# Kernel tuning notes

Hardware: AMD Instinct MI355X
Metric: run time of the kernel (lower is better)

## Reference

```python
import jax, jax.numpy as jnp
import numpy as np

CUBE_SIZE = 3
RADIUS = 0.25
NSAMPLE = 512
B, N = 128, 8192


def make_centers():
    # grid of cube_size^3 centers, centered at origin, spacing = radius
    g = np.arange(CUBE_SIZE, dtype=np.float32)
    c = np.stack(np.meshgrid(g, g, g, indexing='ij'), axis=-1).reshape(-1, 3)
    c -= (CUBE_SIZE - 1) / 2.0
    c *= RADIUS
    return jnp.asarray(c[None])  # [1, P, 3]


def setup_inputs() -> dict:
    key = jax.random.key(0)
    xyz = jax.random.normal(key, (B, N, 3), dtype=jnp.float32)
    return {"xyz": xyz, "centers": make_centers()}


def reference(xyz, centers):
    # xyz: [B, N, 3], centers: [1, P, 3]
    b_, n_, _ = xyz.shape
    p_ = centers.shape[1]
    c = jnp.broadcast_to(centers, (b_, p_, 3))

    # squared distances [B, P, N] without materializing [B,P,N,3]
    x2 = jnp.sum(xyz * xyz, axis=-1)            # [B, N]
    c2 = jnp.sum(c * c, axis=-1)                # [B, P]
    xc = jnp.einsum('bpd,bnd->bpn', c, xyz)     # [B, P, N]
    dist2 = x2[:, None, :] + c2[:, :, None] - 2.0 * xc

    # ball query: first NSAMPLE points (in index order) with dist2 < r^2;
    # remaining slots padded with the first found index (0 if none found),
    # matching the PointNet++ CUDA kernel semantics.
    mask = dist2 < (RADIUS * RADIUS)
    order = jnp.where(mask, jnp.cumsum(mask, axis=-1) - 1, NSAMPLE)  # slot per point
    first_idx = jnp.argmax(mask, axis=-1)                             # [B, P], 0 if none
    idx = jnp.broadcast_to(first_idx[..., None], (b_, p_, NSAMPLE))
    bi = jnp.arange(b_)[:, None, None]
    pi = jnp.arange(p_)[None, :, None]
    js = jnp.broadcast_to(jnp.arange(n_)[None, None, :], (b_, p_, n_))
    idx = idx.at[bi, pi, order].set(js, mode='drop')                  # [B, P, NSAMPLE]

    # gather neighbors and re-center (QueryAndGroup with use_xyz, no features)
    grouped = jnp.take_along_axis(xyz[:, None, :, :], idx[..., None], axis=2)  # [B,P,S,3]
    grouped = grouped - c[:, :, None, :]

    # permute(0,2,3,1) of [B,3,P,S] -> [B,P,S,3] then merge batch and center dims
    return grouped.reshape(b_ * p_, NSAMPLE, 3)
```

## Files before the change

### kernel.cpp

```cpp
#include <hip/hip_runtime.h>


constexpr int P        = 27;
constexpr int N        = 8192;
constexpr int S        = 512;
constexpr int B        = 128;
constexpr int CAND_MAX = 1024;

__global__ __launch_bounds__(256) void pc_fused_kernel(
    const float* __restrict__ xyz, const float* __restrict__ centers,
    float* __restrict__ out) {
  int i   = blockIdx.x;
  int xcd = i & 7;
  int j   = i >> 3;
  int b   = xcd * 16 + j / 7;
  int g   = j % 7;
  int tid = threadIdx.x, lane = tid & 63, wave = tid >> 6;

  __shared__ float4 s_cand[CAND_MAX];
  __shared__ int    s_wsum[4];

  const float* pts = xyz + (size_t)b * (N * 3);

  const float4* p4 = (const float4*)pts + (size_t)tid * 24;
  unsigned mask = 0;
#pragma unroll
  for (int grp = 0; grp < 4; ++grp) {
    float4 f[6];
#pragma unroll
    for (int k = 0; k < 6; ++k) f[k] = p4[grp * 6 + k];
    const float* fp = (const float*)f;
#pragma unroll
    for (int k = 0; k < 8; ++k) {
      float x = fp[3 * k + 0], y = fp[3 * k + 1], z = fp[3 * k + 2];
      float cx = fminf(fmaxf(roundf(x * 4.0f), -1.0f), 1.0f) * 0.25f;
      float cy = fminf(fmaxf(roundf(y * 4.0f), -1.0f), 1.0f) * 0.25f;
      float cz = fminf(fmaxf(roundf(z * 4.0f), -1.0f), 1.0f) * 0.25f;
      float dx = x - cx, dy = y - cy, dz = z - cz;
      float d2 = dx * dx + dy * dy + dz * dz;
      if (d2 < 0.0625f + 1e-4f) mask |= 1u << (grp * 8 + k);
    }
  }

  int pcnt = __popc(mask);
  int incl = pcnt;
#pragma unroll
  for (int d = 1; d < 64; d <<= 1) {
    int v = __shfl_up(incl, d);
    if (lane >= d) incl += v;
  }
  if (lane == 63) s_wsum[wave] = incl;
  __syncthreads();
  int woff = 0, ctot = 0;
#pragma unroll
  for (int w = 0; w < 4; ++w) {
    int c = s_wsum[w];
    if (w < wave) woff += c;
    ctot += c;
  }
  int pos = woff + (incl - pcnt);
  unsigned mm = mask;
  while (mm) {
    int k = __ffs(mm) - 1;
    mm &= mm - 1;
    if (pos < CAND_MAX) {
      int n = tid * 32 + k;
      s_cand[pos] = make_float4(pts[n * 3], pts[n * 3 + 1], pts[n * 3 + 2], 0.f);
    }
    ++pos;
  }
  __syncthreads();

  int p = g * 4 + wave;
  if (p >= P) return;

  float cx = centers[p * 3 + 0];
  float cy = centers[p * 3 + 1];
  float cz = centers[p * 3 + 2];
  double cxd = (double)cx, cyd = (double)cy, czd = (double)cz;
  float* o = out + ((size_t)b * P + p) * (S * 3);

  int base = 0;
  bool has_first = false;
  float f0x = 0.f, f0y = 0.f, f0z = 0.f;
  if (ctot <= CAND_MAX) {
    for (int off = 0; off < ctot && base < S; off += 64) {
      int idx  = off + lane;
      bool act = idx < ctot;
      float4 pt = act ? s_cand[idx] : make_float4(0.f, 0.f, 0.f, 0.f);
      double dx = (double)pt.x - cxd;
      double dy = (double)pt.y - cyd;
      double dz = (double)pt.z - czd;
      bool inball = act && (dx * dx + dy * dy + dz * dz < 0.0625);
      unsigned long long m = __ballot(inball);
      int slot = base + __popcll(m & ((1ull << lane) - 1ull));
      if (inball && slot < S) {
        float fx = pt.x - cx, fy = pt.y - cy, fz = pt.z - cz;
        o[slot * 3 + 0] = fx;
        o[slot * 3 + 1] = fy;
        o[slot * 3 + 2] = fz;
        if (slot == 0) { has_first = true; f0x = fx; f0y = fy; f0z = fz; }
      }
      base += __popcll(m);
    }
  } else {
    for (int off = 0; off < N && base < S; off += 64) {
      int n = off + lane;
      float x = pts[n * 3 + 0], y = pts[n * 3 + 1], z = pts[n * 3 + 2];
      double dx = (double)x - cxd, dy = (double)y - cyd, dz = (double)z - czd;
      bool inball = dx * dx + dy * dy + dz * dz < 0.0625;
      unsigned long long m = __ballot(inball);
      int slot = base + __popcll(m & ((1ull << lane) - 1ull));
      if (inball && slot < S) {
        float fx = x - cx, fy = y - cy, fz = z - cz;
        o[slot * 3 + 0] = fx;
        o[slot * 3 + 1] = fy;
        o[slot * 3 + 2] = fz;
        if (slot == 0) { has_first = true; f0x = fx; f0y = fy; f0z = fz; }
      }
      base += __popcll(m);
    }
  }

  float px, py, pz;
  unsigned long long fm = __ballot(has_first);
  if (fm) {
    int src = __ffsll((unsigned long long)fm) - 1;
    px = __shfl(f0x, src); py = __shfl(f0y, src); pz = __shfl(f0z, src);
  } else {
    px = pts[0] - cx; py = pts[1] - cy; pz = pts[2] - cz;
  }

  int filled = base < S ? base : S;
  int d0 = filled * 3;
  int hb = (d0 + 3) & ~3;
  if (hb > 1536) hb = 1536;
  if (lane < hb - d0) {
    int d = d0 + lane;
    int rr = d % 3;
    o[d] = rr == 0 ? px : (rr == 1 ? py : pz);
  }
  for (int gq = (hb >> 2) + lane; gq < 1536 / 4; gq += 64) {
    int rr = gq % 3;
    float a  = rr == 0 ? px : (rr == 1 ? py : pz);
    float b2 = rr == 0 ? py : (rr == 1 ? pz : px);
    float c2 = rr == 0 ? pz : (rr == 1 ? px : py);
    ((float4*)o)[gq] = make_float4(a, b2, c2, a);
  }
}

extern "C" void kernel_launch(void* const* d_in, const int* in_sizes, int n_in,
                              void* d_out, int out_size, void* d_ws, size_t ws_size,
                              hipStream_t stream) {
  const float* xyz     = (const float*)d_in[0];
  const float* centers = (const float*)d_in[1];
  float* out           = (float*)d_out;
  (void)d_ws; (void)ws_size;
  pc_fused_kernel<<<B * 7, 256, 0, stream>>>(xyz, centers, out);
}
```

Before: 85.80 us.

## Compact candidates per-wave segments with ballot, removing block scan and global re-reads

Candidate filtering changes from per-thread 32-point bitmasks plus a block-wide scan into four per-wave segments of 2048 points each. Each wave compacts its in-range candidates with ballot/popcount into its own shared-memory segment, prefetching the next point. This removes the shuffle scan, one barrier and the scattered global re-reads of candidate coordinates. In exchange it uses strided scalar loads instead of float4 loads, has a per-segment cap of 512, and the query phase now walks four segments in order.

Result: faster. 81.79 us (-4.7%).

```diff
diff --git a/kernel.cpp b/kernel.cpp
--- a/kernel.cpp
+++ b/kernel.cpp
@@ -1,11 +1,12 @@
 #include <hip/hip_runtime.h>
 
 
-constexpr int P        = 27;
-constexpr int N        = 8192;
-constexpr int S        = 512;
-constexpr int B        = 128;
-constexpr int CAND_MAX = 1024;
+constexpr int P      = 27;
+constexpr int N      = 8192;
+constexpr int S      = 512;
+constexpr int B      = 128;
+constexpr int SEGPTS = 2048;
+constexpr int SEGCAP = 512;
 
 __global__ __launch_bounds__(256) void pc_fused_kernel(
     const float* __restrict__ xyz, const float* __restrict__ centers,
@@ -17,59 +18,45 @@
   int g   = j % 7;
   int tid = threadIdx.x, lane = tid & 63, wave = tid >> 6;
 
-  __shared__ float4 s_cand[CAND_MAX];
-  __shared__ int    s_wsum[4];
+  __shared__ float4 s_cand[4 * SEGCAP];
+  __shared__ int    s_wcnt[4];
 
   const float* pts = xyz + (size_t)b * (N * 3);
 
-  const float4* p4 = (const float4*)pts + (size_t)tid * 24;
-  unsigned mask = 0;
-#pragma unroll
-  for (int grp = 0; grp < 4; ++grp) {
-    float4 f[6];
-#pragma unroll
-    for (int k = 0; k < 6; ++k) f[k] = p4[grp * 6 + k];
-    const float* fp = (const float*)f;
-#pragma unroll
-    for (int k = 0; k < 8; ++k) {
-      float x = fp[3 * k + 0], y = fp[3 * k + 1], z = fp[3 * k + 2];
+  {
+    const float* sp = pts + wave * (SEGPTS * 3);
+    float4* seg = s_cand + wave * SEGCAP;
+    unsigned long long lmask = (1ull << lane) - 1ull;
+
+    int i3 = lane * 3;
+    float x = sp[i3], y = sp[i3 + 1], z = sp[i3 + 2];
+    int cnt = 0;
+    for (int it = 0; it < SEGPTS / 64; ++it) {
+      float nx = 0.f, ny = 0.f, nz = 0.f;
+      if (it < SEGPTS / 64 - 1) {
+        int n3 = ((it + 1) * 64 + lane) * 3;
+        nx = sp[n3]; ny = sp[n3 + 1]; nz = sp[n3 + 2];
+      }
       float cx = fminf(fmaxf(roundf(x * 4.0f), -1.0f), 1.0f) * 0.25f;
       float cy = fminf(fmaxf(roundf(y * 4.0f), -1.0f), 1.0f) * 0.25f;
       float cz = fminf(fmaxf(roundf(z * 4.0f), -1.0f), 1.0f) * 0.25f;
       float dx = x - cx, dy = y - cy, dz = z - cz;
-      float d2 = dx * dx + dy * dy + dz * dz;
-      if (d2 < 0.0625f + 1e-4f) mask |= 1u << (grp * 8 + k);
+      bool keep = (dx * dx + dy * dy + dz * dz) < (0.0625f + 1e-4f);
+
+      unsigned long long m = __ballot(keep);
+      if (keep) {
+        int pos = cnt + __popcll(m & lmask);
+        if (pos < SEGCAP) seg[pos] = make_float4(x, y, z, 0.0f);
+      }
+      cnt += __popcll(m);
+      x = nx; y = ny; z = nz;
     }
-  }
-
-  int pcnt = __popc(mask);
-  int incl = pcnt;
-#pragma unroll
-  for (int d = 1; d < 64; d <<= 1) {
-    int v = __shfl_up(incl, d);
-    if (lane >= d) incl += v;
-  }
-  if (lane == 63) s_wsum[wave] = incl;
-  __syncthreads();
-  int woff = 0, ctot = 0;
-#pragma unroll
-  for (int w = 0; w < 4; ++w) {
-    int c = s_wsum[w];
-    if (w < wave) woff += c;
-    ctot += c;
-  }
-  int pos = woff + (incl - pcnt);
-  unsigned mm = mask;
-  while (mm) {
-    int k = __ffs(mm) - 1;
-    mm &= mm - 1;
-    if (pos < CAND_MAX) {
-      int n = tid * 32 + k;
-      s_cand[pos] = make_float4(pts[n * 3], pts[n * 3 + 1], pts[n * 3 + 2], 0.f);
-    }
-    ++pos;
+    if (lane == 0) s_wcnt[wave] = cnt;
   }
   __syncthreads();
+
+  int c0 = s_wcnt[0], c1 = s_wcnt[1], c2 = s_wcnt[2], c3 = s_wcnt[3];
+  bool ovf = (c0 > SEGCAP) | (c1 > SEGCAP) | (c2 > SEGCAP) | (c3 > SEGCAP);
 
   int p = g * 4 + wave;
   if (p >= P) return;
@@ -79,29 +66,36 @@
   float cz = centers[p * 3 + 2];
   double cxd = (double)cx, cyd = (double)cy, czd = (double)cz;
   float* o = out + ((size_t)b * P + p) * (S * 3);
+  unsigned long long lmask = (1ull << lane) - 1ull;
 
   int base = 0;
   bool has_first = false;
   float f0x = 0.f, f0y = 0.f, f0z = 0.f;
-  if (ctot <= CAND_MAX) {
-    for (int off = 0; off < ctot && base < S; off += 64) {
-      int idx  = off + lane;
-      bool act = idx < ctot;
-      float4 pt = act ? s_cand[idx] : make_float4(0.f, 0.f, 0.f, 0.f);
-      double dx = (double)pt.x - cxd;
-      double dy = (double)pt.y - cyd;
-      double dz = (double)pt.z - czd;
-      bool inball = act && (dx * dx + dy * dy + dz * dz < 0.0625);
-      unsigned long long m = __ballot(inball);
-      int slot = base + __popcll(m & ((1ull << lane) - 1ull));
-      if (inball && slot < S) {
-        float fx = pt.x - cx, fy = pt.y - cy, fz = pt.z - cz;
-        o[slot * 3 + 0] = fx;
-        o[slot * 3 + 1] = fy;
-        o[slot * 3 + 2] = fz;
-        if (slot == 0) { has_first = true; f0x = fx; f0y = fy; f0z = fz; }
+  if (!ovf) {
+    int segcnt[4] = {c0, c1, c2, c3};
+#pragma unroll
+    for (int q = 0; q < 4; ++q) {
+      const float4* seg = s_cand + q * SEGCAP;
+      int cnt = segcnt[q];
+      for (int off = 0; off < cnt && base < S; off += 64) {
+        int idx  = off + lane;
+        bool act = idx < cnt;
+        float4 pt = act ? seg[idx] : make_float4(0.f, 0.f, 0.f, 0.f);
+        double dx = (double)pt.x - cxd;
+        double dy = (double)pt.y - cyd;
+        double dz = (double)pt.z - czd;
+        bool inball = act && (dx * dx + dy * dy + dz * dz < 0.0625);
+        unsigned long long m = __ballot(inball);
+        int slot = base + __popcll(m & lmask);
+        if (inball && slot < S) {
+          float fx = pt.x - cx, fy = pt.y - cy, fz = pt.z - cz;
+          o[slot * 3 + 0] = fx;
+          o[slot * 3 + 1] = fy;
+          o[slot * 3 + 2] = fz;
+          if (slot == 0) { has_first = true; f0x = fx; f0y = fy; f0z = fz; }
+        }
+        base += __popcll(m);
       }
-      base += __popcll(m);
     }
   } else {
     for (int off = 0; off < N && base < S; off += 64) {
@@ -110,7 +104,7 @@
       double dx = (double)x - cxd, dy = (double)y - cyd, dz = (double)z - czd;
       bool inball = dx * dx + dy * dy + dz * dz < 0.0625;
       unsigned long long m = __ballot(inball);
-      int slot = base + __popcll(m & ((1ull << lane) - 1ull));
+      int slot = base + __popcll(m & lmask);
       if (inball && slot < S) {
         float fx = x - cx, fy = y - cy, fz = z - cz;
         o[slot * 3 + 0] = fx;
```
